# Optimization experiments

Measured on AMD Instinct MI355X. Metric: run time of the kernel, lower is better.

## Reference

```python
import jax, jax.numpy as jnp
import numpy as np

NUM_HEADS = 16
HEAD_DIM = 128  # d_out // num_heads
D_IN = 2048
D_OUT = 2048
B = 2
T = 2048
W_SCALE = 0.02  # keep softmax logits in a sane range


def setup_inputs() -> dict:
    key = jax.random.key(0)
    ks = jax.random.split(key, 6)
    x = jax.random.normal(ks[0], (B, T, D_IN), dtype=jnp.float32)
    Wq = jax.random.normal(ks[1], (D_OUT, D_IN), dtype=jnp.float32) * W_SCALE
    Wk = jax.random.normal(ks[2], (HEAD_DIM, D_IN), dtype=jnp.float32) * W_SCALE
    Wv = jax.random.normal(ks[3], (HEAD_DIM, D_IN), dtype=jnp.float32) * W_SCALE
    Wo = jax.random.normal(ks[4], (D_OUT, D_OUT), dtype=jnp.float32) * W_SCALE
    bo = jnp.zeros((D_OUT,), dtype=jnp.float32)
    return {"x": x, "Wq": Wq, "Wk": Wk, "Wv": Wv, "Wo": Wo, "bo": bo}


def reference(x, Wq, Wk, Wv, Wo, bo):
    b, t, _ = x.shape
    # projections (torch nn.Linear: y = x @ W.T)
    q = jnp.einsum('btd,ed->bte', x, Wq).reshape(b, t, NUM_HEADS, HEAD_DIM)
    q = q.transpose(0, 2, 1, 3)                      # [b, H, T, hd]
    k = jnp.einsum('btd,ed->bte', x, Wk)             # [b, T, hd] single KV head
    v = jnp.einsum('btd,ed->bte', x, Wv)             # [b, T, hd]
    # MQA: single K/V head broadcast across all query heads
    scale = 1.0 / jnp.sqrt(jnp.float32(HEAD_DIM))
    scores = jnp.einsum('bhqd,bkd->bhqk', q, k) * scale  # [b, H, T, T]
    # NOTE: the original module computes a causal mask but never applies it,
    # so attention is unmasked (faithful to source).
    w = jax.nn.softmax(scores, axis=-1)
    ctx = jnp.einsum('bhqk,bkd->bhqd', w, v)         # [b, H, T, hd]
    ctx = ctx.transpose(0, 2, 1, 3).reshape(b, t, D_OUT)
    return jnp.einsum('btd,ed->bte', ctx, Wo) + bo
```

## Files before the change

kernel.cpp:

```cpp
#include <hip/hip_runtime.h>

typedef unsigned short u16;
typedef unsigned int   u32;
typedef __bf16 bf16x8 __attribute__((ext_vector_type(8)));
typedef float  f32x4  __attribute__((ext_vector_type(4)));
typedef u32    u32x2  __attribute__((ext_vector_type(2)));

constexpr int TB   = 2;
constexpr int TT   = 2048;
constexpr int DIN  = 2048;
constexpr int DOUT = 2048;
constexpr int NH   = 16;
constexpr int HD   = 128;
constexpr int MR   = TB * TT;
constexpr int NQKV = DOUT + 2 * HD;

constexpr float QSC = 0.08838834764831845f * 1.4426950408889634f;

__device__ __forceinline__ u16 f2b(float f) {
  return __builtin_bit_cast(u16, (__bf16)f);
}

__global__ __launch_bounds__(256) void k_cast_all(const float* __restrict__ x,
                                                  const float* __restrict__ wq,
                                                  const float* __restrict__ wk,
                                                  const float* __restrict__ wv,
                                                  const float* __restrict__ wo,
                                                  u16* __restrict__ xb,
                                                  u16* __restrict__ wqkv,
                                                  u16* __restrict__ wob) {
  int bid = blockIdx.x;
  const float* s; u16* d; int base;
  if (bid < 8192)       { s = x;  d = xb;   base = bid; }
  else if (bid < 12288) { s = wq; d = wqkv; base = bid - 8192; }
  else if (bid < 12544) { s = wk; d = wqkv + (size_t)DOUT * DIN;        base = bid - 12288; }
  else if (bid < 12800) { s = wv; d = wqkv + (size_t)(DOUT + HD) * DIN; base = bid - 12544; }
  else                  { s = wo; d = wob;  base = bid - 12800; }
  int i = (base * 256 + threadIdx.x) * 4;
  float4 v = *(const float4*)(s + i);
  ushort4 o;
  o.x = f2b(v.x); o.y = f2b(v.y); o.z = f2b(v.z); o.w = f2b(v.w);
  *(ushort4*)(d + i) = o;
}

__device__ __forceinline__ void async16(const u16* g, u16* l) {
  __builtin_amdgcn_global_load_lds((const __attribute__((address_space(1))) void*)g,
                                   (__attribute__((address_space(3))) void*)l,
                                   16, 0, 0);
}

template<bool F32OUT>
__global__ __launch_bounds__(512) void k_gemm(const u16* __restrict__ A,
                                              const u16* __restrict__ Bm,
                                              void* __restrict__ Cv,
                                              const float* __restrict__ bias,
                                              int M, int N, int K) {
  __shared__ u16 lA[2][128 * 64];
  __shared__ u16 lB[2][128 * 64];
  const int tid = threadIdx.x;
  const int w = tid >> 6, l = tid & 63;
  const int wr = w >> 1, wc = w & 1;
  const int r16 = l & 15, kq = l >> 4;

  int nwg = gridDim.x * gridDim.y;
  int wg = blockIdx.y * gridDim.x + blockIdx.x;
  if ((nwg & 7) == 0) wg = (wg & 7) * (nwg >> 3) + (wg >> 3);
  const int rowS = (wg / gridDim.x) * 128, colS = (wg % gridDim.x) * 128;

  const int srow = tid >> 3, scol = (tid & 7) * 8;

  auto stage = [&](int buf, int k0) {
#pragma unroll
    for (int i = 0; i < 2; ++i) {
      int e = i * 512 + tid;
      async16(A  + (size_t)(rowS + srow + i * 64) * K + k0 + scol, &lA[buf][e * 8]);
      async16(Bm + (size_t)(colS + srow + i * 64) * K + k0 + scol, &lB[buf][e * 8]);
    }
  };

  f32x4 acc[2][4] = {};

  stage(0, 0);
  asm volatile("s_waitcnt vmcnt(0)" ::: "memory");
  __syncthreads();

  int cur = 0;
  for (int k0 = 0; k0 < K; k0 += 64) {
    if (k0 + 64 < K) stage(cur ^ 1, k0 + 64);
#pragma unroll
    for (int kk = 0; kk < 2; ++kk) {
      bf16x8 af[2], bfr[4];
#pragma unroll
      for (int m = 0; m < 2; ++m)
        af[m] = *(const bf16x8*)&lA[cur][(wr * 32 + m * 16 + r16) * 64 + kk * 32 + kq * 8];
#pragma unroll
      for (int n = 0; n < 4; ++n)
        bfr[n] = *(const bf16x8*)&lB[cur][(wc * 64 + n * 16 + r16) * 64 + kk * 32 + kq * 8];
      __builtin_amdgcn_s_setprio(1);
#pragma unroll
      for (int m = 0; m < 2; ++m)
#pragma unroll
        for (int n = 0; n < 4; ++n)
          acc[m][n] = __builtin_amdgcn_mfma_f32_16x16x32_bf16(af[m], bfr[n], acc[m][n], 0, 0, 0);
      __builtin_amdgcn_s_setprio(0);
    }
    asm volatile("s_waitcnt vmcnt(0)" ::: "memory");
    __syncthreads();
    cur ^= 1;
  }

#pragma unroll
  for (int m = 0; m < 2; ++m)
#pragma unroll
    for (int n = 0; n < 4; ++n)
#pragma unroll
      for (int j = 0; j < 4; ++j) {
        int r = rowS + wr * 32 + m * 16 + kq * 4 + j;
        int c = colS + wc * 64 + n * 16 + r16;
        if constexpr (F32OUT) {
          ((float*)Cv)[(size_t)r * N + c] = acc[m][n][j] + bias[c];
        } else {
          float v = acc[m][n][j];
          if (c < DOUT) v *= QSC;
          ((u16*)Cv)[(size_t)r * N + c] = f2b(v);
        }
      }
}

__global__ __launch_bounds__(256) void k_transpose_v(const u16* __restrict__ qkv,
                                                     u16* __restrict__ vtg) {
  __shared__ u16 tile[64 * 136];
  const int blk = blockIdx.x;
  const int b = blk / (TT / 64), t0 = (blk % (TT / 64)) * 64;
  const int tid = threadIdx.x;
#pragma unroll
  for (int i = 0; i < 4; ++i) {
    int e = i * 256 + tid;
    int row = e >> 4, col = (e & 15) * 8;
    *(uint4*)&tile[row * 136 + col] =
        *(const uint4*)(qkv + (size_t)(b * TT + t0 + row) * NQKV + DOUT + HD + col);
  }
  __syncthreads();
#pragma unroll
  for (int i = 0; i < 4; ++i) {
    int e = i * 256 + tid;
    int d = e >> 3, tc = (e & 7) * 8;
    u16 tmp[8];
#pragma unroll
    for (int j = 0; j < 8; ++j) tmp[j] = tile[(tc + j) * 136 + d];
    *(uint4*)(vtg + ((size_t)b * HD + d) * TT + t0 + tc) = *(uint4*)tmp;
  }
}

#define KT_IDX(r, c) ((r) * 128 + ((c) ^ (((r) & 7) << 3)))
#define VT_IDX(r, c) ((r) * 64 + ((c) ^ (((r) & 7) << 3)))

__global__ __launch_bounds__(512) void k_attn(const u16* __restrict__ qkv,
                                              const u16* __restrict__ vtg,
                                              u16* __restrict__ ctxg) {
  __shared__ u16 Kt[2][64 * 128];
  __shared__ u16 Vt[2][128 * 64];
  __shared__ u16 Pt[8][16 * 40];

  const int qt = blockIdx.x, h = blockIdx.y, b = blockIdx.z;
  const int tid = threadIdx.x, w = tid >> 6, l = tid & 63;
  const int r16 = l & 15, kq = l >> 4;
  const int q0 = qt * 128 + w * 16;
  const size_t rowbase = (size_t)b * TT;

  bf16x8 qf[4];
  const u16* qrow = qkv + (rowbase + q0 + r16) * NQKV + h * HD + kq * 8;
#pragma unroll
  for (int kk = 0; kk < 4; ++kk) qf[kk] = *(const bf16x8*)(qrow + kk * 32);

  const int krow0 = tid >> 4, kcol = (tid & 15) * 8;
  const int vrow0 = tid >> 3, vcol = (tid & 7) * 8;
  const u16* kglob = qkv + (rowbase)*NQKV + DOUT;
  const u16* vglob = vtg + (size_t)b * HD * TT;

  uint4 kr0, kr1, vr0, vr1;
  auto load_tiles = [&](int kv0) {
    const u16* kb = kglob + (size_t)kv0 * NQKV;
    kr0 = *(const uint4*)(kb + (size_t)krow0 * NQKV + kcol);
    kr1 = *(const uint4*)(kb + (size_t)(krow0 + 32) * NQKV + kcol);
    const u16* vb = vglob + kv0;
    vr0 = *(const uint4*)(vb + (size_t)vrow0 * TT + vcol);
    vr1 = *(const uint4*)(vb + (size_t)(vrow0 + 64) * TT + vcol);
  };
  auto write_tiles = [&](int buf) {
    *(uint4*)&Kt[buf][KT_IDX(krow0, kcol)]      = kr0;
    *(uint4*)&Kt[buf][KT_IDX(krow0 + 32, kcol)] = kr1;
    *(uint4*)&Vt[buf][VT_IDX(vrow0, vcol)]      = vr0;
    *(uint4*)&Vt[buf][VT_IDX(vrow0 + 64, vcol)] = vr1;
  };

  f32x4 ctx[8] = {};
  float l_run = 0.0f;

  load_tiles(0);
  write_tiles(0);
  __syncthreads();

  for (int t = 0; t < TT / 64; ++t) {
    const int cur = t & 1;
    if (t < TT / 64 - 1) load_tiles((t + 1) * 64);

    f32x4 s[4] = {};
#pragma unroll
    for (int n = 0; n < 4; ++n) {
      bf16x8 kf[4];
#pragma unroll
      for (int kk = 0; kk < 4; ++kk)
        kf[kk] = *(const bf16x8*)&Kt[cur][KT_IDX(n * 16 + r16, kk * 32 + kq * 8)];
      __builtin_amdgcn_s_setprio(1);
#pragma unroll
      for (int kk = 0; kk < 4; ++kk)
        s[n] = __builtin_amdgcn_mfma_f32_16x16x32_bf16(kf[kk], qf[kk], s[n], 0, 0, 0);
      __builtin_amdgcn_s_setprio(0);
    }

    float rsum = 0.0f;
    float p[4][4];
#pragma unroll
    for (int n = 0; n < 4; ++n)
#pragma unroll
      for (int j = 0; j < 4; ++j) {
        p[n][j] = exp2f(s[n][j]);
        rsum += p[n][j];
      }
    rsum += __shfl_xor(rsum, 16);
    rsum += __shfl_xor(rsum, 32);
    l_run += rsum;

    u32 pk[4][2];
#pragma unroll
    for (int n = 0; n < 4; ++n) {
      pk[n][0] = (u32)f2b(p[n][0]) | ((u32)f2b(p[n][1]) << 16);
      pk[n][1] = (u32)f2b(p[n][2]) | ((u32)f2b(p[n][3]) << 16);
    }

    u16* pw = Pt[w];
#pragma unroll
    for (int hh = 0; hh < 2; ++hh) {
      u32x2 w0, w1;
      w0[0] = pk[2 * hh][0];     w0[1] = pk[2 * hh][1];
      w1[0] = pk[2 * hh + 1][0]; w1[1] = pk[2 * hh + 1][1];
      *(u32x2*)&pw[r16 * 40 + kq * 4]      = w0;
      *(u32x2*)&pw[r16 * 40 + 16 + kq * 4] = w1;
      bf16x8 pf = *(const bf16x8*)&pw[r16 * 40 + kq * 8];
      __builtin_amdgcn_s_setprio(1);
#pragma unroll
      for (int f = 0; f < 8; ++f) {
        bf16x8 vf = *(const bf16x8*)&Vt[cur][VT_IDX(f * 16 + r16, hh * 32 + kq * 8)];
        ctx[f] = __builtin_amdgcn_mfma_f32_16x16x32_bf16(vf, pf, ctx[f], 0, 0, 0);
      }
      __builtin_amdgcn_s_setprio(0);
    }

    if (t < TT / 64 - 1) write_tiles(cur ^ 1);
    __syncthreads();
  }

  const float inv = 1.0f / l_run;
  u16* crow = ctxg + (rowbase + q0 + r16) * DOUT + h * HD + kq * 4;
#pragma unroll
  for (int f = 0; f < 8; ++f) {
    u32x2 o;
    o[0] = (u32)f2b(ctx[f][0] * inv) | ((u32)f2b(ctx[f][1] * inv) << 16);
    o[1] = (u32)f2b(ctx[f][2] * inv) | ((u32)f2b(ctx[f][3] * inv) << 16);
    *(u32x2*)(crow + f * 16) = o;
  }
}

extern "C" void kernel_launch(void* const* d_in, const int* in_sizes, int n_in,
                              void* d_out, int out_size, void* d_ws, size_t ws_size,
                              hipStream_t stream) {
  const float* x  = (const float*)d_in[0];
  const float* Wq = (const float*)d_in[1];
  const float* Wk = (const float*)d_in[2];
  const float* Wv = (const float*)d_in[3];
  const float* Wo = (const float*)d_in[4];
  const float* bo = (const float*)d_in[5];
  float* out = (float*)d_out;

  char* ws = (char*)d_ws;
  u16* xb   = (u16*)(ws + 0);
  u16* wqkv = (u16*)(ws + 16777216);
  u16* wo   = (u16*)(ws + 26214400);
  u16* qkv  = (u16*)(ws + 34603008);
  u16* vtg  = (u16*)(ws + 53477376);
  u16* ctx  = (u16*)(ws + 54525952);

  k_cast_all<<<16896, 256, 0, stream>>>(x, Wq, Wk, Wv, Wo, xb, wqkv, wo);

  k_gemm<false><<<dim3(NQKV / 128, MR / 128), 512, 0, stream>>>(
      xb, wqkv, (void*)qkv, nullptr, MR, NQKV, DIN);

  k_transpose_v<<<TB * TT / 64, 256, 0, stream>>>(qkv, vtg);

  k_attn<<<dim3(TT / 128, NH, TB), 512, 0, stream>>>(qkv, vtg, ctx);

  k_gemm<true><<<dim3(DOUT / 128, MR / 128), 512, 0, stream>>>(
      ctx, wo, (void*)out, bo, MR, DOUT, DOUT);
}
```

Before: 346.5 us.

## Enlarge GEMM tiles to 256x256 with XOR-swizzled LDS and interleaved staging

Replaces the 128x128 GEMM with a 256x256-tile kernel where each of 8 waves computes a 128x64 sub-tile. It XOR-swizzles the LDS layout to avoid bank conflicts and splits the next-tile prefetch into A and B halves interleaved between MFMA phases with barriers. The goal is more data reuse per LDS load and less global traffic per FLOP. In exchange it raises register pressure, doubles LDS to 128KB, and yields fewer workgroups (e.g. 144 for the QKV GEMM), which may underfill 256 CUs.

```diff
diff --git a/kernel.cpp b/kernel.cpp
--- a/kernel.cpp
+++ b/kernel.cpp
@@ -49,73 +49,104 @@
                                    16, 0, 0);
 }
 
+#define GPH(MH, KK, BFV, LOADB, STMT)                                                       \
+  {                                                                                         \
+    bf16x8 af[4];                                                                           \
+    const char* baA = (const char*)&lA[cur][0];                                             \
+    const char* baB = (const char*)&lB[cur][0];                                             \
+    const int cso = (((KK) * 4 + kq) ^ sw) << 4;                                            \
+    _Pragma("unroll")                                                                       \
+    for (int mm = 0; mm < 4; ++mm)                                                          \
+      af[mm] = *(const bf16x8*)(baA + (wr * 128 + ((MH) * 4 + mm) * 16 + r16) * 128 + cso); \
+    if (LOADB) {                                                                            \
+      _Pragma("unroll")                                                                     \
+      for (int n = 0; n < 4; ++n)                                                           \
+        BFV[n] = *(const bf16x8*)(baB + (wc * 64 + n * 16 + r16) * 128 + cso);              \
+    }                                                                                       \
+    STMT;                                                                                   \
+    __builtin_amdgcn_s_barrier();                                                           \
+    __builtin_amdgcn_s_setprio(1);                                                          \
+    _Pragma("unroll")                                                                       \
+    for (int mm = 0; mm < 4; ++mm)                                                          \
+      _Pragma("unroll")                                                                     \
+      for (int n = 0; n < 4; ++n)                                                           \
+        acc[(MH) * 4 + mm][n] = __builtin_amdgcn_mfma_f32_16x16x32_bf16(                    \
+            af[mm], BFV[n], acc[(MH) * 4 + mm][n], 0, 0, 0);                                \
+    __builtin_amdgcn_s_setprio(0);                                                          \
+    __builtin_amdgcn_s_barrier();                                                           \
+  }
+
 template<bool F32OUT>
-__global__ __launch_bounds__(512) void k_gemm(const u16* __restrict__ A,
-                                              const u16* __restrict__ Bm,
-                                              void* __restrict__ Cv,
-                                              const float* __restrict__ bias,
-                                              int M, int N, int K) {
-  __shared__ u16 lA[2][128 * 64];
-  __shared__ u16 lB[2][128 * 64];
+__global__ __launch_bounds__(512, 2) void k_gemm8(const u16* __restrict__ A,
+                                                  const u16* __restrict__ Bm,
+                                                  void* __restrict__ Cv,
+                                                  const float* __restrict__ bias,
+                                                  int M, int N, int K) {
+  __shared__ u16 lA[2][256 * 64];
+  __shared__ u16 lB[2][256 * 64];
   const int tid = threadIdx.x;
   const int w = tid >> 6, l = tid & 63;
-  const int wr = w >> 1, wc = w & 1;
+  const int wr = w >> 2, wc = w & 3;
   const int r16 = l & 15, kq = l >> 4;
+  const int sw = r16 & 7;
 
   int nwg = gridDim.x * gridDim.y;
   int wg = blockIdx.y * gridDim.x + blockIdx.x;
   if ((nwg & 7) == 0) wg = (wg & 7) * (nwg >> 3) + (wg >> 3);
-  const int rowS = (wg / gridDim.x) * 128, colS = (wg % gridDim.x) * 128;
-
-  const int srow = tid >> 3, scol = (tid & 7) * 8;
-
-  auto stage = [&](int buf, int k0) {
-#pragma unroll
-    for (int i = 0; i < 2; ++i) {
+  const int rowS = (wg / gridDim.x) * 256, colS = (wg % gridDim.x) * 256;
+
+  auto stageA = [&](int buf, int k0) {
+#pragma unroll
+    for (int i = 0; i < 4; ++i) {
       int e = i * 512 + tid;
-      async16(A  + (size_t)(rowS + srow + i * 64) * K + k0 + scol, &lA[buf][e * 8]);
-      async16(Bm + (size_t)(colS + srow + i * 64) * K + k0 + scol, &lB[buf][e * 8]);
+      int row = e >> 3;
+      int gc = ((e & 7) ^ (row & 7)) * 8;
+      async16(A + (size_t)(rowS + row) * K + k0 + gc, &lA[buf][e * 8]);
     }
   };
-
-  f32x4 acc[2][4] = {};
-
-  stage(0, 0);
+  auto stageB = [&](int buf, int k0) {
+#pragma unroll
+    for (int i = 0; i < 4; ++i) {
+      int e = i * 512 + tid;
+      int row = e >> 3;
+      int gc = ((e & 7) ^ (row & 7)) * 8;
+      async16(Bm + (size_t)(colS + row) * K + k0 + gc, &lB[buf][e * 8]);
+    }
+  };
+
+  f32x4 acc[8][4] = {};
+
+  stageA(0, 0);
+  stageB(0, 0);
   asm volatile("s_waitcnt vmcnt(0)" ::: "memory");
   __syncthreads();
 
+  const int NT = K >> 6;
   int cur = 0;
-  for (int k0 = 0; k0 < K; k0 += 64) {
-    if (k0 + 64 < K) stage(cur ^ 1, k0 + 64);
-#pragma unroll
-    for (int kk = 0; kk < 2; ++kk) {
-      bf16x8 af[2], bfr[4];
-#pragma unroll
-      for (int m = 0; m < 2; ++m)
-        af[m] = *(const bf16x8*)&lA[cur][(wr * 32 + m * 16 + r16) * 64 + kk * 32 + kq * 8];
-#pragma unroll
-      for (int n = 0; n < 4; ++n)
-        bfr[n] = *(const bf16x8*)&lB[cur][(wc * 64 + n * 16 + r16) * 64 + kk * 32 + kq * 8];
-      __builtin_amdgcn_s_setprio(1);
-#pragma unroll
-      for (int m = 0; m < 2; ++m)
-#pragma unroll
-        for (int n = 0; n < 4; ++n)
-          acc[m][n] = __builtin_amdgcn_mfma_f32_16x16x32_bf16(af[m], bfr[n], acc[m][n], 0, 0, 0);
-      __builtin_amdgcn_s_setprio(0);
-    }
-    asm volatile("s_waitcnt vmcnt(0)" ::: "memory");
-    __syncthreads();
+  for (int t = 0; t < NT; ++t) {
+    const int k0n = (t + 1) << 6;
+    const bool pre = (t + 1 < NT);
+    bf16x8 bf0[4], bf1[4];
+
+    GPH(0, 0, bf0, true,  { if (pre) stageA(cur ^ 1, k0n); });
+    GPH(1, 0, bf0, false, { if (pre) stageB(cur ^ 1, k0n); });
+    GPH(0, 1, bf1, true,  {});
+    GPH(1, 1, bf1, false, {});
+
+    if (pre) {
+      asm volatile("s_waitcnt vmcnt(0)" ::: "memory");
+      __builtin_amdgcn_s_barrier();
+    }
     cur ^= 1;
   }
 
 #pragma unroll
-  for (int m = 0; m < 2; ++m)
+  for (int m = 0; m < 8; ++m)
 #pragma unroll
     for (int n = 0; n < 4; ++n)
 #pragma unroll
       for (int j = 0; j < 4; ++j) {
-        int r = rowS + wr * 32 + m * 16 + kq * 4 + j;
+        int r = rowS + wr * 128 + m * 16 + kq * 4 + j;
         int c = colS + wc * 64 + n * 16 + r16;
         if constexpr (F32OUT) {
           ((float*)Cv)[(size_t)r * N + c] = acc[m][n][j] + bias[c];
@@ -293,13 +324,13 @@
 
   k_cast_all<<<16896, 256, 0, stream>>>(x, Wq, Wk, Wv, Wo, xb, wqkv, wo);
 
-  k_gemm<false><<<dim3(NQKV / 128, MR / 128), 512, 0, stream>>>(
+  k_gemm8<false><<<dim3(NQKV / 256, MR / 256), 512, 0, stream>>>(
       xb, wqkv, (void*)qkv, nullptr, MR, NQKV, DIN);
 
   k_transpose_v<<<TB * TT / 64, 256, 0, stream>>>(qkv, vtg);
 
   k_attn<<<dim3(TT / 128, NH, TB), 512, 0, stream>>>(qkv, vtg, ctx);
 
-  k_gemm<true><<<dim3(DOUT / 128, MR / 128), 512, 0, stream>>>(
+  k_gemm8<true><<<dim3(DOUT / 256, MR / 256), 512, 0, stream>>>(
       ctx, wo, (void*)out, bo, MR, DOUT, DOUT);
 }
```

After: 326.7 us. 1.06x faster.
